# Kernel tuning notes

Hardware: AMD Instinct MI355X
Metric: run time of the kernel (lower is better)

The kernel has to match this reference:

```python
import jax, jax.numpy as jnp
import numpy as np

NUM_HEADS = 16
HEAD_DIM = 64
HIDDEN = NUM_HEADS * HEAD_DIM  # 1024


def get_rel_pos(q_size, k_size, rel_pos):
    # q_size == k_size here and rel_pos already has 2*size-1 rows, so the
    # F.interpolate(mode='linear') resize in the original is an identity.
    # relative_coords = q - k + (k_size - 1)  (scale factors are 1.0)
    coords = jnp.arange(q_size)[:, None] - jnp.arange(k_size)[None, :] + (k_size - 1)
    return rel_pos[coords]  # [q_size, k_size, head_dim]


def setup_inputs() -> dict:
    key = jax.random.key(0)
    ks = jax.random.split(key, 7)
    B, H, W = 4, 56, 28
    inp = {
        "hidden_states": jax.random.normal(ks[0], (B, H, W, HIDDEN), jnp.float32),
        "qkv_w": jax.random.normal(ks[1], (3 * HIDDEN, HIDDEN), jnp.float32) * 0.02,
        "qkv_b": jax.random.normal(ks[2], (3 * HIDDEN,), jnp.float32) * 0.02,
        "proj_w": jax.random.normal(ks[3], (HIDDEN, HIDDEN), jnp.float32) * 0.02,
        "proj_b": jax.random.normal(ks[4], (HIDDEN,), jnp.float32) * 0.02,
        "rel_pos_h": jax.random.normal(ks[5], (2 * H - 1, HEAD_DIM), jnp.float32) * 0.02,
        "rel_pos_w": jax.random.normal(ks[6], (2 * W - 1, HEAD_DIM), jnp.float32) * 0.02,
    }
    return inp


def reference(hidden_states, qkv_w, qkv_b, proj_w, proj_b, rel_pos_h, rel_pos_w):
    B, H, W, C = hidden_states.shape
    N = H * W
    scale = HEAD_DIM ** -0.5

    # qkv projection -> [3, B*heads, N, head_dim]
    qkv = hidden_states @ qkv_w.T + qkv_b
    qkv = qkv.reshape(B, N, 3, NUM_HEADS, HEAD_DIM).transpose(2, 0, 3, 1, 4)
    qkv = qkv.reshape(3, B * NUM_HEADS, N, HEAD_DIM)
    query, key_, value = qkv[0], qkv[1], qkv[2]

    # scaled dot-product scores, fully materialized as in the original
    attn = jnp.einsum('bqd,bkd->bqk', query * scale, key_)  # [B*heads, N, N]

    # decomposed relative position bias
    Rh = get_rel_pos(H, H, rel_pos_h)  # [H, H, d]
    Rw = get_rel_pos(W, W, rel_pos_w)  # [W, W, d]
    q_r = query.reshape(B * NUM_HEADS, H, W, HEAD_DIM)
    rel_h = jnp.einsum('bhwc,hkc->bhwk', q_r, Rh)  # [B*heads, H, W, H]
    rel_w = jnp.einsum('bhwc,wkc->bhwk', q_r, Rw)  # [B*heads, H, W, W]
    attn = attn.reshape(B * NUM_HEADS, H, W, H, W)
    attn = attn + rel_h[:, :, :, :, None] + rel_w[:, :, :, None, :]
    attn = attn.reshape(B * NUM_HEADS, N, N)

    attn = jax.nn.softmax(attn.astype(jnp.float32), axis=-1).astype(query.dtype)

    out = jnp.einsum('bqk,bkd->bqd', attn, value)
    out = out.reshape(B, NUM_HEADS, H, W, HEAD_DIM).transpose(0, 2, 3, 1, 4)
    out = out.reshape(B, H, W, C)
    out = out @ proj_w.T + proj_b
    return out
```

## Files before the change

kernel.cpp:

```cpp
#include <hip/hip_runtime.h>
#include <hip/hip_bf16.h>
#include <stdint.h>

typedef __bf16 bf16;
typedef __bf16 bf16x2 __attribute__((ext_vector_type(2)));
typedef __bf16 bf16x4 __attribute__((ext_vector_type(4)));
typedef __bf16 bf16x8 __attribute__((ext_vector_type(8)));
typedef float f32x4 __attribute__((ext_vector_type(4)));

#define AS1 __attribute__((address_space(1)))
#define AS3 __attribute__((address_space(3)))

static __device__ __forceinline__ float b2f(bf16 x) { return (float)x; }

static __device__ __forceinline__ void async_cp16(const bf16* g, bf16* l) {
    __builtin_amdgcn_global_load_lds((const AS1 void*)g, (AS3 void*)l, 16, 0, 0);
}

static __device__ __forceinline__ bf16x4 cvt4(f32x4 v) {
    bf16x4 r;
    r[0] = (bf16)v[0]; r[1] = (bf16)v[1]; r[2] = (bf16)v[2]; r[3] = (bf16)v[3];
    return r;
}

static __device__ __forceinline__ float fast_exp2(float x) {
#if __has_builtin(__builtin_amdgcn_exp2f)
    return __builtin_amdgcn_exp2f(x);
#else
    return __expf(x * 0.69314718056f);
#endif
}

__global__ __launch_bounds__(256) void cvt3_kernel(
    const float* __restrict__ a, const float* __restrict__ b,
    const float* __restrict__ c, bf16* __restrict__ dst,
    int na4, int nb4, int ntot4) {
    int i = blockIdx.x * 256 + threadIdx.x;
    const int stride = gridDim.x * 256;
    for (; i < ntot4; i += stride) {
        f32x4 v;
        if (i < na4)            v = ((const f32x4*)a)[i];
        else if (i < na4 + nb4) v = ((const f32x4*)b)[i - na4];
        else                    v = ((const f32x4*)c)[i - na4 - nb4];
        ((bf16x4*)dst)[i] = cvt4(v);
    }
}


#define QKV_EPILOGUE()                                                        \
    for (int nt = 0; nt < 4; nt++) {                                          \
        const int n_ = n0 + wn + nt * 16 + lm;                                \
        const float bv = bias[n_];                                            \
        const int s = n_ >> 10, rem = n_ & 1023;                              \
        const int h = rem >> 6, d = rem & 63;                                 \
        for (int mt = 0; mt < 4; mt++) {                                      \
            for (int r = 0; r < 4; r++) {                                     \
                const int m_ = m0 + wm + mt * 16 + quad * 4 + r;              \
                const int b = m_ / 1568;                                      \
                const int pix = m_ - b * 1568;                                \
                const int g = b * 16 + h;                                     \
                const bf16 v = (bf16)(acc[mt][nt][r] + bv);                   \
                if (s == 0)      Qb[((size_t)g * 1568 + pix) * 64 + d] = v;   \
                else if (s == 1) Kb[((size_t)g * 1568 + pix) * 64 + d] = v;   \
                else {                                                        \
                    const int lk = pix & 31;                                  \
                    const int ppix = (pix & ~31) | ((lk & 15) << 1) | (lk >> 4); \
                    Vt[((size_t)g * 64 + d) * 1568 + ppix] = v;               \
                }                                                             \
            }                                                                 \
        }                                                                     \
    }

__global__ __launch_bounds__(256) void qkv_gemm_bf16(
    const bf16* __restrict__ A, const bf16* __restrict__ W,
    const float* __restrict__ bias, bf16* __restrict__ Qb,
    bf16* __restrict__ Kb, bf16* __restrict__ Vt) {
    __shared__ bf16 As[128 * 32];
    __shared__ bf16 Bs[128 * 32];
    const int t = threadIdx.x;
    const int wid = t >> 6, lane = t & 63;
    const int m0 = blockIdx.x * 128, n0 = blockIdx.y * 128;
    const int wm = (wid & 1) * 64, wn = (wid >> 1) * 64;
    const int r_i = lane >> 2, c8 = (lane & 3) * 8;
    const int lm = lane & 15, quad = lane >> 4;

    f32x4 acc[4][4] = {};
    for (int k0 = 0; k0 < 1024; k0 += 32) {
        __syncthreads();
        for (int i = 0; i < 2; i++) {
            const int blk = wid * 2 + i;
            async_cp16(A + (size_t)(m0 + blk * 16 + r_i) * 1024 + k0 + c8, As + blk * 512);
            async_cp16(W + (size_t)(n0 + blk * 16 + r_i) * 1024 + k0 + c8, Bs + blk * 512);
        }
        __syncthreads();
        bf16x8 af[4], bfr[4];
        for (int x = 0; x < 4; x++) {
            af[x]  = *(const bf16x8*)&As[(wm + x * 16 + lm) * 32 + quad * 8];
            bfr[x] = *(const bf16x8*)&Bs[(wn + x * 16 + lm) * 32 + quad * 8];
        }
        for (int mt = 0; mt < 4; mt++)
            for (int nt = 0; nt < 4; nt++)
                acc[mt][nt] = __builtin_amdgcn_mfma_f32_16x16x32_bf16(af[mt], bfr[nt], acc[mt][nt], 0, 0, 0);
    }
    QKV_EPILOGUE()
}

__global__ __launch_bounds__(256) void qkv_gemm_f32(
    const float* __restrict__ A, const float* __restrict__ W,
    const float* __restrict__ bias, bf16* __restrict__ Qb,
    bf16* __restrict__ Kb, bf16* __restrict__ Vt) {
    __shared__ bf16 As[128 * 32];
    __shared__ bf16 Bs[128 * 32];
    const int t = threadIdx.x;
    const int wid = t >> 6, lane = t & 63;
    const int m0 = blockIdx.x * 128, n0 = blockIdx.y * 128;
    const int wm = (wid & 1) * 64, wn = (wid >> 1) * 64;
    const int lm = lane & 15, quad = lane >> 4;

    f32x4 acc[4][4] = {};
    for (int k0 = 0; k0 < 1024; k0 += 32) {
        __syncthreads();
        for (int i = 0; i < 4; i++) {
            const int idx = t + i * 256;
            const int row = idx >> 3, c4 = (idx & 7) * 4;
            const f32x4 av = *(const f32x4*)&A[(size_t)(m0 + row) * 1024 + k0 + c4];
            const f32x4 wv = *(const f32x4*)&W[(size_t)(n0 + row) * 1024 + k0 + c4];
            *(bf16x4*)&As[row * 32 + c4] = cvt4(av);
            *(bf16x4*)&Bs[row * 32 + c4] = cvt4(wv);
        }
        __syncthreads();
        bf16x8 af[4], bfr[4];
        for (int x = 0; x < 4; x++) {
            af[x]  = *(const bf16x8*)&As[(wm + x * 16 + lm) * 32 + quad * 8];
            bfr[x] = *(const bf16x8*)&Bs[(wn + x * 16 + lm) * 32 + quad * 8];
        }
        for (int mt = 0; mt < 4; mt++)
            for (int nt = 0; nt < 4; nt++)
                acc[mt][nt] = __builtin_amdgcn_mfma_f32_16x16x32_bf16(af[mt], bfr[nt], acc[mt][nt], 0, 0, 0);
    }
    QKV_EPILOGUE()
}

__global__ __launch_bounds__(256) void flash_attn(
    const bf16* __restrict__ Qb, const bf16* __restrict__ Kb,
    const bf16* __restrict__ Vt, const float* __restrict__ rph,
    const float* __restrict__ rpw, bf16* __restrict__ AO) {
    const int x = blockIdx.x;
    const int xcd = x & 7, j = x >> 3;
    const int g = xcd * 8 + j / 25;
    const int qblk = j - (j / 25) * 25;
    const int q0 = qblk * 64;

    __shared__ __align__(16) char smem[47104];
    bf16* Th  = (bf16*)smem;
    bf16* Tw  = (bf16*)(smem + 14592);
    char* B   = smem + 22016;
    bf16* Qs  = (bf16*)B;
    bf16* RPs = (bf16*)B;
    bf16* Ks  = (bf16*)B;
    bf16* Vts = (bf16*)(B + 4608);
    bf16* Ps  = (bf16*)(B + 14848);

    const int t = threadIdx.x, wid = t >> 6, lane = t & 63;
    const int lm = lane & 15, quad = lane >> 4;
    const int qbase_l = wid * 16 + quad * 4;

    for (int c = t; c < 512; c += 256) {
        const int row = c >> 3, col = (c & 7) * 8;
        const int qg = min(q0 + row, 1567);
        *(bf16x8*)&Qs[row * 72 + col] =
            *(const bf16x8*)&Qb[((size_t)g * 1568 + qg) * 64 + col];
    }
    __syncthreads();
    const int qrow_l = wid * 16 + lm;
    const bf16x8 qf0 = *(const bf16x8*)&Qs[qrow_l * 72 + quad * 8];
    const bf16x8 qf1 = *(const bf16x8*)&Qs[qrow_l * 72 + 32 + quad * 8];
    int thb[4], twb[4];
#pragma unroll
    for (int r = 0; r < 4; r++) {
        const int qg = min(q0 + qbase_l + r, 1567);
        const int hq = qg / 28;
        thb[r] = (qbase_l + r) * 114 + hq + 55;
        twb[r] = (qbase_l + r) * 58 + (qg - hq * 28) + 27;
    }
    __syncthreads();

    for (int c = t; c < 1776; c += 256) {
        const int row = c >> 4, col = (c & 15) * 4;
        *(bf16x4*)&RPs[row * 72 + col] = cvt4(*(const f32x4*)&rph[row * 64 + col]);
    }
    __syncthreads();
    f32x4 acch[7];
#pragma unroll
    for (int nt = 0; nt < 7; nt++) {
        const bf16x8 b0 = *(const bf16x8*)&RPs[(nt * 16 + lm) * 72 + quad * 8];
        const bf16x8 b1 = *(const bf16x8*)&RPs[(nt * 16 + lm) * 72 + 32 + quad * 8];
        f32x4 a = {};
        a = __builtin_amdgcn_mfma_f32_16x16x32_bf16(qf0, b0, a, 0, 0, 0);
        a = __builtin_amdgcn_mfma_f32_16x16x32_bf16(qf1, b1, a, 0, 0, 0);
        acch[nt] = a;
    }
    __syncthreads();

    for (int c = t; c < 880; c += 256) {
        const int row = c >> 4, col = (c & 15) * 4;
        *(bf16x4*)&RPs[row * 72 + col] = cvt4(*(const f32x4*)&rpw[row * 64 + col]);
    }
#pragma unroll
    for (int nt = 0; nt < 7; nt++)
#pragma unroll
        for (int r = 0; r < 4; r++)
            Th[(qbase_l + r) * 114 + nt * 16 + lm] = (bf16)(acch[nt][r] * 8.0f);
    __syncthreads();
#pragma unroll
    for (int nt = 0; nt < 4; nt++) {
        const bf16x8 b0 = *(const bf16x8*)&RPs[(nt * 16 + lm) * 72 + quad * 8];
        const bf16x8 b1 = *(const bf16x8*)&RPs[(nt * 16 + lm) * 72 + 32 + quad * 8];
        f32x4 a = {};
        a = __builtin_amdgcn_mfma_f32_16x16x32_bf16(qf0, b0, a, 0, 0, 0);
        a = __builtin_amdgcn_mfma_f32_16x16x32_bf16(qf1, b1, a, 0, 0, 0);
        const int col = nt * 16 + lm;
        if (col < 58) {
#pragma unroll
            for (int r = 0; r < 4; r++)
                Tw[(qbase_l + r) * 58 + col] = (bf16)(a[r] * 8.0f);
        }
    }

    f32x4 o[4] = {};
    float l_lane[4] = {0.f, 0.f, 0.f, 0.f};
    const float C2 = 0.125f * 1.44269504f;
    const float S2 = 10.0f * 1.44269504f;

    const int ks_k = t >> 3, ks_d = (t & 7) * 8;
    const int vs_d = t >> 2, vs_k = (t & 3) * 8;

    int hk0 = 0, wk0 = lm;
    int hk1 = (16 + lm) >= 28 ? 1 : 0;
    int wk1 = 16 + lm - (hk1 ? 28 : 0);

    const size_t kgbase = ((size_t)g * 1568 + ks_k) * 64 + ks_d;
    const size_t vgbase = ((size_t)g * 64 + vs_d) * 1568 + vs_k;
    bf16x8 kreg = *(const bf16x8*)&Kb[kgbase];
    bf16x8 vreg = *(const bf16x8*)&Vt[vgbase];

    for (int kt = 0; kt < 49; kt++) {
        const int vb = kt & 1;
        f32x4 s0, s1;
#pragma unroll
        for (int r = 0; r < 4; r++) {
            s0[r] = b2f(Th[thb[r] - hk0]) + b2f(Tw[twb[r] - wk0]);
            s1[r] = b2f(Th[thb[r] - hk1]) + b2f(Tw[twb[r] - wk1]);
        }
        wk0 += 4; hk0 += 1; if (wk0 >= 28) { wk0 -= 28; hk0 += 1; }
        wk1 += 4; hk1 += 1; if (wk1 >= 28) { wk1 -= 28; hk1 += 1; }

        __syncthreads();
        *(bf16x8*)&Ks[ks_k * 72 + ks_d] = kreg;
        *(bf16x8*)&Vts[vb * 2560 + vs_d * 40 + vs_k] = vreg;
        {
            const int ktn = min(kt + 1, 48);
            kreg = *(const bf16x8*)&Kb[kgbase + (size_t)ktn * 2048];
            vreg = *(const bf16x8*)&Vt[vgbase + ktn * 32];
        }

        if (kt) {
            const int ob = vb ^ 1;
            const bf16x8 pf = *(const bf16x8*)&Ps[ob * 2560 + wid * 640 + lm * 40 + quad * 8];
#pragma unroll
            for (int dt = 0; dt < 4; dt++) {
                const bf16x8 vf = *(const bf16x8*)&Vts[ob * 2560 + (dt * 16 + lm) * 40 + quad * 8];
                o[dt] = __builtin_amdgcn_mfma_f32_16x16x32_bf16(pf, vf, o[dt], 0, 0, 0);
            }
        }
        __syncthreads();

        {
            const bf16x8 ka0 = *(const bf16x8*)&Ks[lm * 72 + quad * 8];
            const bf16x8 ka1 = *(const bf16x8*)&Ks[lm * 72 + 32 + quad * 8];
            s0 = __builtin_amdgcn_mfma_f32_16x16x32_bf16(qf0, ka0, s0, 0, 0, 0);
            s0 = __builtin_amdgcn_mfma_f32_16x16x32_bf16(qf1, ka1, s0, 0, 0, 0);
            const bf16x8 kb0 = *(const bf16x8*)&Ks[(16 + lm) * 72 + quad * 8];
            const bf16x8 kb1 = *(const bf16x8*)&Ks[(16 + lm) * 72 + 32 + quad * 8];
            s1 = __builtin_amdgcn_mfma_f32_16x16x32_bf16(qf0, kb0, s1, 0, 0, 0);
            s1 = __builtin_amdgcn_mfma_f32_16x16x32_bf16(qf1, kb1, s1, 0, 0, 0);
        }

        bf16* Pw = &Ps[vb * 2560 + wid * 640];
#pragma unroll
        for (int r = 0; r < 4; r++) {
            const float p0 = fast_exp2(fmaf(s0[r], C2, -S2));
            const float p1 = fast_exp2(fmaf(s1[r], C2, -S2));
            l_lane[r] += p0 + p1;
            bf16x2 pp; pp[0] = (bf16)p0; pp[1] = (bf16)p1;
            *(bf16x2*)&Pw[(quad * 4 + r) * 40 + lm * 2] = pp;
        }
    }

    __asm__ volatile("s_waitcnt lgkmcnt(0)" ::: "memory");
    {
        const bf16x8 pf = *(const bf16x8*)&Ps[wid * 640 + lm * 40 + quad * 8];
#pragma unroll
        for (int dt = 0; dt < 4; dt++) {
            const bf16x8 vf = *(const bf16x8*)&Vts[(dt * 16 + lm) * 40 + quad * 8];
            o[dt] = __builtin_amdgcn_mfma_f32_16x16x32_bf16(pf, vf, o[dt], 0, 0, 0);
        }
    }

    const int qrow0 = q0 + qbase_l;
    if (q0 + wid * 16 < 1568) {
        const int bo = g >> 4, h = g & 15;
#pragma unroll
        for (int r = 0; r < 4; r++) {
            float ll = l_lane[r];
            for (int off = 1; off < 16; off <<= 1) ll += __shfl_xor(ll, off, 64);
            const float inv = 1.0f / ll;
            const size_t base = ((size_t)bo * 1568 + qrow0 + r) * 1024 + h * 64;
            for (int dt = 0; dt < 4; dt++)
                AO[base + dt * 16 + lm] = (bf16)(o[dt][r] * inv);
        }
    }
}

__global__ __launch_bounds__(256) void proj_gemm_bf16(
    const bf16* __restrict__ A, const bf16* __restrict__ W,
    const float* __restrict__ bias, float* __restrict__ out) {
    __shared__ bf16 As[128 * 32];
    __shared__ bf16 Bs[128 * 32];
    const int t = threadIdx.x;
    const int wid = t >> 6, lane = t & 63;
    const int m0 = blockIdx.x * 128, n0 = blockIdx.y * 128;
    const int wm = (wid & 1) * 64, wn = (wid >> 1) * 64;
    const int r_i = lane >> 2, c8 = (lane & 3) * 8;
    const int lm = lane & 15, quad = lane >> 4;

    f32x4 acc[4][4] = {};
    for (int k0 = 0; k0 < 1024; k0 += 32) {
        __syncthreads();
        for (int i = 0; i < 2; i++) {
            const int blk = wid * 2 + i;
            async_cp16(A + (size_t)(m0 + blk * 16 + r_i) * 1024 + k0 + c8, As + blk * 512);
            async_cp16(W + (size_t)(n0 + blk * 16 + r_i) * 1024 + k0 + c8, Bs + blk * 512);
        }
        __syncthreads();
        bf16x8 af[4], bfr[4];
        for (int x = 0; x < 4; x++) {
            af[x]  = *(const bf16x8*)&As[(wm + x * 16 + lm) * 32 + quad * 8];
            bfr[x] = *(const bf16x8*)&Bs[(wn + x * 16 + lm) * 32 + quad * 8];
        }
        for (int mt = 0; mt < 4; mt++)
            for (int nt = 0; nt < 4; nt++)
                acc[mt][nt] = __builtin_amdgcn_mfma_f32_16x16x32_bf16(af[mt], bfr[nt], acc[mt][nt], 0, 0, 0);
    }
    for (int nt = 0; nt < 4; nt++) {
        const int n_ = n0 + wn + nt * 16 + lm;
        const float bv = bias[n_];
        for (int mt = 0; mt < 4; mt++)
            for (int r = 0; r < 4; r++) {
                const int m_ = m0 + wm + mt * 16 + quad * 4 + r;
                out[(size_t)m_ * 1024 + n_] = acc[mt][nt][r] + bv;
            }
    }
}

__global__ __launch_bounds__(256) void proj_gemm_f32(
    const bf16* __restrict__ A, const float* __restrict__ W,
    const float* __restrict__ bias, float* __restrict__ out) {
    __shared__ bf16 As[128 * 32];
    __shared__ bf16 Bs[128 * 32];
    const int t = threadIdx.x;
    const int wid = t >> 6, lane = t & 63;
    const int m0 = blockIdx.x * 128, n0 = blockIdx.y * 128;
    const int wm = (wid & 1) * 64, wn = (wid >> 1) * 64;
    const int r_i = lane >> 2, c8 = (lane & 3) * 8;
    const int lm = lane & 15, quad = lane >> 4;

    f32x4 acc[4][4] = {};
    for (int k0 = 0; k0 < 1024; k0 += 32) {
        __syncthreads();
        for (int i = 0; i < 2; i++) {
            const int blk = wid * 2 + i;
            async_cp16(A + (size_t)(m0 + blk * 16 + r_i) * 1024 + k0 + c8, As + blk * 512);
        }
        for (int i = 0; i < 4; i++) {
            const int idx = t + i * 256;
            const int row = idx >> 3, c4 = (idx & 7) * 4;
            const f32x4 wv = *(const f32x4*)&W[(size_t)(n0 + row) * 1024 + k0 + c4];
            *(bf16x4*)&Bs[row * 32 + c4] = cvt4(wv);
        }
        __syncthreads();
        bf16x8 af[4], bfr[4];
        for (int x = 0; x < 4; x++) {
            af[x]  = *(const bf16x8*)&As[(wm + x * 16 + lm) * 32 + quad * 8];
            bfr[x] = *(const bf16x8*)&Bs[(wn + x * 16 + lm) * 32 + quad * 8];
        }
        for (int mt = 0; mt < 4; mt++)
            for (int nt = 0; nt < 4; nt++)
                acc[mt][nt] = __builtin_amdgcn_mfma_f32_16x16x32_bf16(af[mt], bfr[nt], acc[mt][nt], 0, 0, 0);
    }
    for (int nt = 0; nt < 4; nt++) {
        const int n_ = n0 + wn + nt * 16 + lm;
        const float bv = bias[n_];
        for (int mt = 0; mt < 4; mt++)
            for (int r = 0; r < 4; r++) {
                const int m_ = m0 + wm + mt * 16 + quad * 4 + r;
                out[(size_t)m_ * 1024 + n_] = acc[mt][nt][r] + bv;
            }
    }
}

extern "C" void kernel_launch(void* const* d_in, const int* in_sizes, int n_in,
                              void* d_out, int out_size, void* d_ws, size_t ws_size,
                              hipStream_t stream) {
    const float* hs     = (const float*)d_in[0];
    const float* qkv_w  = (const float*)d_in[1];
    const float* qkv_b  = (const float*)d_in[2];
    const float* proj_w = (const float*)d_in[3];
    const float* proj_b = (const float*)d_in[4];
    const float* rph    = (const float*)d_in[5];
    const float* rpw    = (const float*)d_in[6];
    float* out = (float*)d_out;

    const size_t GQ = (size_t)64 * 1568 * 64;
    const size_t N_HS = (size_t)6272 * 1024;
    const size_t N_QW = (size_t)3072 * 1024;
    const size_t N_PW = (size_t)1024 * 1024;
    bf16* Qb = (bf16*)d_ws;
    bf16* Kb = Qb + GQ;
    bf16* Vt = Kb + GQ;
    bf16* AO = Vt + GQ;
    bf16* hs_bf    = AO + GQ;
    bf16* qkvw_bf  = hs_bf + N_HS;
    bf16* projw_bf = qkvw_bf + N_QW;
    const size_t need = (4 * GQ + N_HS + N_QW + N_PW) * sizeof(bf16);

    if (ws_size >= need) {
        cvt3_kernel<<<1024, 256, 0, stream>>>(hs, qkv_w, proj_w, hs_bf,
                                              (int)(N_HS / 4), (int)(N_QW / 4),
                                              (int)((N_HS + N_QW + N_PW) / 4));
        qkv_gemm_bf16<<<dim3(49, 24), 256, 0, stream>>>(hs_bf, qkvw_bf, qkv_b, Qb, Kb, Vt);
        flash_attn<<<1600, 256, 0, stream>>>(Qb, Kb, Vt, rph, rpw, AO);
        proj_gemm_bf16<<<dim3(49, 8), 256, 0, stream>>>(AO, projw_bf, proj_b, out);
    } else {
        qkv_gemm_f32<<<dim3(49, 24), 256, 0, stream>>>(hs, qkv_w, qkv_b, Qb, Kb, Vt);
        flash_attn<<<1600, 256, 0, stream>>>(Qb, Kb, Vt, rph, rpw, AO);
        proj_gemm_f32<<<dim3(49, 8), 256, 0, stream>>>(AO, proj_w, proj_b, out);
    }
}
```

Baseline: 357.8 us.

## Load K/V fragments directly from global into registers, drop LDS staging and barriers

The attention loop no longer stages K and V tiles through shared memory. Each wave loads its MFMA operand fragments straight from global memory into registers, prefetching the next tile, and runs the PV MFMA in the same iteration using only a per-wave P buffer. This removes two block-wide barriers per iteration and cuts LDS use, which may raise occupancy. In exchange each of the four waves reloads the same K/V data, so global/L2 traffic grows about fourfold, and the V loads are strided less coalesced accesses.

```diff
diff --git a/kernel.cpp b/kernel.cpp
--- a/kernel.cpp
+++ b/kernel.cpp
@@ -151,15 +151,13 @@
     const int qblk = j - (j / 25) * 25;
     const int q0 = qblk * 64;
 
-    __shared__ __align__(16) char smem[47104];
+    __shared__ __align__(16) char smem[38144];
     bf16* Th  = (bf16*)smem;
     bf16* Tw  = (bf16*)(smem + 14592);
     char* B   = smem + 22016;
     bf16* Qs  = (bf16*)B;
     bf16* RPs = (bf16*)B;
-    bf16* Ks  = (bf16*)B;
-    bf16* Vts = (bf16*)(B + 4608);
-    bf16* Ps  = (bf16*)(B + 14848);
+    bf16* Ps  = (bf16*)B;
 
     const int t = threadIdx.x, wid = t >> 6, lane = t & 63;
     const int lm = lane & 15, quad = lane >> 4;
@@ -226,26 +224,44 @@
                 Tw[(qbase_l + r) * 58 + col] = (bf16)(a[r] * 8.0f);
         }
     }
+    __syncthreads();
 
     f32x4 o[4] = {};
     float l_lane[4] = {0.f, 0.f, 0.f, 0.f};
     const float C2 = 0.125f * 1.44269504f;
     const float S2 = 10.0f * 1.44269504f;
 
-    const int ks_k = t >> 3, ks_d = (t & 7) * 8;
-    const int vs_d = t >> 2, vs_k = (t & 3) * 8;
-
     int hk0 = 0, wk0 = lm;
     int hk1 = (16 + lm) >= 28 ? 1 : 0;
     int wk1 = 16 + lm - (hk1 ? 28 : 0);
 
-    const size_t kgbase = ((size_t)g * 1568 + ks_k) * 64 + ks_d;
-    const size_t vgbase = ((size_t)g * 64 + vs_d) * 1568 + vs_k;
-    bf16x8 kreg = *(const bf16x8*)&Kb[kgbase];
-    bf16x8 vreg = *(const bf16x8*)&Vt[vgbase];
+    bf16* Pw = &Ps[wid * 640];
+
+    const bf16* kbase = Kb + ((size_t)g * 1568 + lm) * 64 + quad * 8;
+    const bf16* vbase = Vt + ((size_t)g * 64 + lm) * 1568 + quad * 8;
+
+    bf16x8 ka0c = *(const bf16x8*)(kbase);
+    bf16x8 ka1c = *(const bf16x8*)(kbase + 32);
+    bf16x8 kb0c = *(const bf16x8*)(kbase + 1024);
+    bf16x8 kb1c = *(const bf16x8*)(kbase + 1056);
+    bf16x8 v0c = *(const bf16x8*)(vbase);
+    bf16x8 v1c = *(const bf16x8*)(vbase + 16 * 1568);
+    bf16x8 v2c = *(const bf16x8*)(vbase + 32 * 1568);
+    bf16x8 v3c = *(const bf16x8*)(vbase + 48 * 1568);
 
     for (int kt = 0; kt < 49; kt++) {
-        const int vb = kt & 1;
+        const int ktn = min(kt + 1, 48);
+        const bf16* kn = kbase + (size_t)ktn * 2048;
+        const bf16* vn = vbase + ktn * 32;
+        const bf16x8 ka0n = *(const bf16x8*)(kn);
+        const bf16x8 ka1n = *(const bf16x8*)(kn + 32);
+        const bf16x8 kb0n = *(const bf16x8*)(kn + 1024);
+        const bf16x8 kb1n = *(const bf16x8*)(kn + 1056);
+        const bf16x8 v0n = *(const bf16x8*)(vn);
+        const bf16x8 v1n = *(const bf16x8*)(vn + 16 * 1568);
+        const bf16x8 v2n = *(const bf16x8*)(vn + 32 * 1568);
+        const bf16x8 v3n = *(const bf16x8*)(vn + 48 * 1568);
+
         f32x4 s0, s1;
 #pragma unroll
         for (int r = 0; r < 4; r++) {
@@ -255,38 +271,11 @@
         wk0 += 4; hk0 += 1; if (wk0 >= 28) { wk0 -= 28; hk0 += 1; }
         wk1 += 4; hk1 += 1; if (wk1 >= 28) { wk1 -= 28; hk1 += 1; }
 
-        __syncthreads();
-        *(bf16x8*)&Ks[ks_k * 72 + ks_d] = kreg;
-        *(bf16x8*)&Vts[vb * 2560 + vs_d * 40 + vs_k] = vreg;
-        {
-            const int ktn = min(kt + 1, 48);
-            kreg = *(const bf16x8*)&Kb[kgbase + (size_t)ktn * 2048];
-            vreg = *(const bf16x8*)&Vt[vgbase + ktn * 32];
-        }
-
-        if (kt) {
-            const int ob = vb ^ 1;
-            const bf16x8 pf = *(const bf16x8*)&Ps[ob * 2560 + wid * 640 + lm * 40 + quad * 8];
-#pragma unroll
-            for (int dt = 0; dt < 4; dt++) {
-                const bf16x8 vf = *(const bf16x8*)&Vts[ob * 2560 + (dt * 16 + lm) * 40 + quad * 8];
-                o[dt] = __builtin_amdgcn_mfma_f32_16x16x32_bf16(pf, vf, o[dt], 0, 0, 0);
-            }
-        }
-        __syncthreads();
-
-        {
-            const bf16x8 ka0 = *(const bf16x8*)&Ks[lm * 72 + quad * 8];
-            const bf16x8 ka1 = *(const bf16x8*)&Ks[lm * 72 + 32 + quad * 8];
-            s0 = __builtin_amdgcn_mfma_f32_16x16x32_bf16(qf0, ka0, s0, 0, 0, 0);
-            s0 = __builtin_amdgcn_mfma_f32_16x16x32_bf16(qf1, ka1, s0, 0, 0, 0);
-            const bf16x8 kb0 = *(const bf16x8*)&Ks[(16 + lm) * 72 + quad * 8];
-            const bf16x8 kb1 = *(const bf16x8*)&Ks[(16 + lm) * 72 + 32 + quad * 8];
-            s1 = __builtin_amdgcn_mfma_f32_16x16x32_bf16(qf0, kb0, s1, 0, 0, 0);
-            s1 = __builtin_amdgcn_mfma_f32_16x16x32_bf16(qf1, kb1, s1, 0, 0, 0);
-        }
-
-        bf16* Pw = &Ps[vb * 2560 + wid * 640];
+        s0 = __builtin_amdgcn_mfma_f32_16x16x32_bf16(qf0, ka0c, s0, 0, 0, 0);
+        s0 = __builtin_amdgcn_mfma_f32_16x16x32_bf16(qf1, ka1c, s0, 0, 0, 0);
+        s1 = __builtin_amdgcn_mfma_f32_16x16x32_bf16(qf0, kb0c, s1, 0, 0, 0);
+        s1 = __builtin_amdgcn_mfma_f32_16x16x32_bf16(qf1, kb1c, s1, 0, 0, 0);
+
 #pragma unroll
         for (int r = 0; r < 4; r++) {
             const float p0 = fast_exp2(fmaf(s0[r], C2, -S2));
@@ -295,16 +284,15 @@
             bf16x2 pp; pp[0] = (bf16)p0; pp[1] = (bf16)p1;
             *(bf16x2*)&Pw[(quad * 4 + r) * 40 + lm * 2] = pp;
         }
-    }
-
-    __asm__ volatile("s_waitcnt lgkmcnt(0)" ::: "memory");
-    {
-        const bf16x8 pf = *(const bf16x8*)&Ps[wid * 640 + lm * 40 + quad * 8];
-#pragma unroll
-        for (int dt = 0; dt < 4; dt++) {
-            const bf16x8 vf = *(const bf16x8*)&Vts[(dt * 16 + lm) * 40 + quad * 8];
-            o[dt] = __builtin_amdgcn_mfma_f32_16x16x32_bf16(pf, vf, o[dt], 0, 0, 0);
-        }
+        __asm__ volatile("s_waitcnt lgkmcnt(0)" ::: "memory");
+        const bf16x8 pf = *(const bf16x8*)&Pw[lm * 40 + quad * 8];
+        o[0] = __builtin_amdgcn_mfma_f32_16x16x32_bf16(pf, v0c, o[0], 0, 0, 0);
+        o[1] = __builtin_amdgcn_mfma_f32_16x16x32_bf16(pf, v1c, o[1], 0, 0, 0);
+        o[2] = __builtin_amdgcn_mfma_f32_16x16x32_bf16(pf, v2c, o[2], 0, 0, 0);
+        o[3] = __builtin_amdgcn_mfma_f32_16x16x32_bf16(pf, v3c, o[3], 0, 0, 0);
+
+        ka0c = ka0n; ka1c = ka1n; kb0c = kb0n; kb1c = kb1n;
+        v0c = v0n; v1c = v1n; v2c = v2n; v3c = v3n;
     }
 
     const int qrow0 = q0 + qbase_l;
```

Result: slower. 456.9 us (+27.7%).
